# Kernel optimization log

Measured on AMD Instinct MI355X. Metric: run time of the kernel, lower is better.

Reference implementation:

```python
import jax, jax.numpy as jnp
import numpy as np

H = 16          # hidden_size
L = 24          # num_layers
LEN_TRAIN = 96
LEN_PRED = 48
B = 256         # leading dim of input (acts as TIME axis for the LSTMs, see notes)


def setup_inputs() -> dict:
    key = jax.random.key(0)
    ks = jax.random.split(key, 16)
    s = 1.0 / np.sqrt(H)  # PyTorch LSTM/Linear init scale
    u = lambda k, shp: jax.random.uniform(k, shp, jnp.float32, -s, s)
    return {
        "x": jax.random.normal(ks[0], (B, 1, LEN_TRAIN), jnp.float32),
        # lstm1: layer0 input_size=1, layers 1..23 input_size=2H
        "W_ih0_1": u(ks[1], (2, 4 * H, 1)),
        "W_ih_1": u(ks[2], (L - 1, 2, 4 * H, 2 * H)),
        "W_hh_1": u(ks[3], (L, 2, 4 * H, H)),
        "b_ih_1": u(ks[4], (L, 2, 4 * H)),
        "b_hh_1": u(ks[5], (L, 2, 4 * H)),
        # lstm2: all layers input_size=2H
        "W_ih_2": u(ks[6], (L, 2, 4 * H, 2 * H)),
        "W_hh_2": u(ks[7], (L, 2, 4 * H, H)),
        "b_ih_2": u(ks[8], (L, 2, 4 * H)),
        "b_hh_2": u(ks[9], (L, 2, 4 * H)),
        "fc1_w": u(ks[10], (1000, 2 * LEN_PRED * H)),
        "fc1_b": u(ks[11], (1000,)),
        "fc2_w": u(ks[12], (LEN_PRED, 1000)),
        "fc2_b": u(ks[13], (LEN_PRED,)),
    }


def _lstm_dir(x, Wih, Whh, bih, bhh, reverse):
    # x: (T, N, in). Precompute input-gate GEMM over whole sequence.
    xg = jnp.einsum("tni,gi->tng", x, Wih) + bih + bhh  # (T, N, 4H)

    def step(carry, g_in):
        h, c = carry
        g = g_in + h @ Whh.T
        i, f, gg, o = jnp.split(g, 4, axis=-1)  # PyTorch gate order i,f,g,o
        c = jax.nn.sigmoid(f) * c + jax.nn.sigmoid(i) * jnp.tanh(gg)
        h = jax.nn.sigmoid(o) * jnp.tanh(c)
        return (h, c), h

    N = x.shape[1]
    init = (jnp.zeros((N, H), x.dtype), jnp.zeros((N, H), x.dtype))
    _, hs = jax.lax.scan(step, init, xg, reverse=reverse)
    return hs  # (T, N, H), in original time order


def _bilstm_stack(x, Wih_per_layer, Whh, bih, bhh):
    for l in range(Whh.shape[0]):
        Wih = Wih_per_layer[l]
        fwd = _lstm_dir(x, Wih[0], Whh[l, 0], bih[l, 0], bhh[l, 0], False)
        bwd = _lstm_dir(x, Wih[1], Whh[l, 1], bih[l, 1], bhh[l, 1], True)
        x = jnp.concatenate([fwd, bwd], axis=-1)  # (T, N, 2H)
    return x


def reference(x, W_ih0_1, W_ih_1, W_hh_1, b_ih_1, b_hh_1,
              W_ih_2, W_hh_2, b_ih_2, b_hh_2,
              fc1_w, fc1_b, fc2_w, fc2_b):
    xp = jnp.transpose(x, (0, 2, 1))  # (B, 96, 1); dim0 is the LSTM time axis (batch_first=False quirk)
    wih1 = [W_ih0_1] + [W_ih_1[i] for i in range(L - 1)]
    h = _bilstm_stack(xp, wih1, W_hh_1, b_ih_1, b_hh_1)      # (B, 96, 2H)
    x1 = h[:, -LEN_PRED:, :]                                  # (B, 48, 2H)
    wih2 = [W_ih_2[i] for i in range(L)]
    h2 = _bilstm_stack(x1, wih2, W_hh_2, b_ih_2, b_hh_2)      # (B, 48, 2H)
    z = h2 + x1
    flat = z.reshape(z.shape[0], -1)                          # (B, 1536)
    y = jax.nn.relu(flat @ fc1_w.T + fc1_b) @ fc2_w.T + fc2_b # (B, 48)
    return jnp.transpose(y.reshape(y.shape[0], LEN_PRED, 1), (0, 2, 1))  # (B, 1, 48)
```

## Files before the change

kernel.cpp:

```cpp
#include <hip/hip_runtime.h>


template <int SEL>
__device__ __forceinline__ float quad_bcast(float v) {
  return __int_as_float(__builtin_amdgcn_update_dpp(
      0, __float_as_int(v), SEL * 0x55, 0xF, 0xF, true));
}

__global__ __launch_bounds__(512) void lstm_fused(
    const float* __restrict__ x, const float* __restrict__ W_ih0_1,
    const float* __restrict__ W_ih_1, const float* __restrict__ W_hh_1,
    const float* __restrict__ b_ih_1, const float* __restrict__ b_hh_1,
    const float* __restrict__ W_ih_2, const float* __restrict__ W_hh_2,
    const float* __restrict__ b_ih_2, const float* __restrict__ b_hh_2,
    float* __restrict__ x1out, float* __restrict__ h2out) {
  __shared__ float xgF[256 * 64];
  __shared__ float xgB[256 * 64];

  const int tid = threadIdx.x;
  const int lane = tid & 63;
  const int w = tid >> 6;
  const int np = blockIdx.x;
  const int nglob = 48 + np;

  {
    const int d = w >> 2;
    const int wv = w & 3;
    float* xg = d ? xgB : xgF;
    const int r = lane;
    const float bias = b_ih_1[d * 64 + r] + b_hh_1[d * 64 + r];
    const float wih0 = W_ih0_1[d * 64 + r];
    const int xvb = __float_as_int(x[(size_t)(wv * 64 + lane) * 96 + nglob]);
    for (int ti = 0; ti < 64; ++ti) {
      const float xs = __int_as_float(__builtin_amdgcn_readlane(xvb, ti));
      xg[(wv * 64 + ti) * 64 + r] = fmaf(wih0, xs, bias);
    }
  }
  __syncthreads();

  for (int L = 0; L < 48; ++L) {
    float wf[32], wb[32];
    float bf0, bf1, bb0, bb1;
    {
      const int M = (L < 47) ? (L + 1) : 47;
      const float* WihP;
      const float* bihP;
      const float* bhhP;
      if (M < 24) {
        WihP = W_ih_1 + (size_t)(M - 1) * 4096;
        bihP = b_ih_1 + (size_t)M * 128;
        bhhP = b_hh_1 + (size_t)M * 128;
      } else {
        WihP = W_ih_2 + (size_t)(M - 24) * 4096;
        bihP = b_ih_2 + (size_t)(M - 24) * 128;
        bhhP = b_hh_2 + (size_t)(M - 24) * 128;
      }
      const int r = lane;
      bf0 = bihP[r];
      bf1 = bhhP[r];
      bb0 = bihP[64 + r];
      bb1 = bhhP[64 + r];
      const float4* pf = reinterpret_cast<const float4*>(WihP + (size_t)r * 32);
      const float4* pb =
          reinterpret_cast<const float4*>(WihP + 2048 + (size_t)r * 32);
#pragma unroll
      for (int q = 0; q < 8; ++q) {
        const float4 a = pf[q];
        wf[4 * q + 0] = a.x;
        wf[4 * q + 1] = a.y;
        wf[4 * q + 2] = a.z;
        wf[4 * q + 3] = a.w;
        const float4 b = pb[q];
        wb[4 * q + 0] = b.x;
        wb[4 * q + 1] = b.y;
        wb[4 * q + 2] = b.z;
        wb[4 * q + 3] = b.w;
      }
    }

    if (w == 0 || w == 5) {
      const int d = (w == 5);
      float* xg = d ? xgB : xgF;
      const int j = lane >> 2;
      const int g = lane & 3;
      const int r = g * 16 + j;

      const float* WhhP = ((L < 24) ? (W_hh_1 + (size_t)L * 2048)
                                    : (W_hh_2 + (size_t)(L - 24) * 2048)) +
                          (size_t)d * 1024 + (size_t)r * 16;
      float whh[16];
#pragma unroll
      for (int k = 0; k < 16; ++k) whh[k] = WhhP[k];

      const float s_ = (g == 2) ? 2.885390082f : -1.442695041f;
      const float m_ = (g == 2) ? -2.0f : 1.0f;
      const float b_ = (g == 2) ? 1.0f : 0.0f;

      float hs[16];
#pragma unroll
      for (int k = 0; k < 16; ++k) hs[k] = 0.f;
      float c = 0.f;

      const int dt = d ? -1 : 1;
      int t = d ? 255 : 0;
      float cur0 = xg[t * 64 + r];
      float cur1 = xg[(t + dt) * 64 + r];

#define LSTM_STEP(CUR, TT)                                                  \
  {                                                                         \
    float a0 = (CUR), a1 = 0.f, a2 = 0.f, a3 = 0.f;                         \
    _Pragma("unroll") for (int k = 0; k < 16; k += 4) {                     \
      a0 = fmaf(whh[k + 0], hs[k + 0], a0);                                 \
      a1 = fmaf(whh[k + 1], hs[k + 1], a1);                                 \
      a2 = fmaf(whh[k + 2], hs[k + 2], a2);                                 \
      a3 = fmaf(whh[k + 3], hs[k + 3], a3);                                 \
    }                                                                       \
    const float gv = (a0 + a1) + (a2 + a3);                                 \
    const float e = __builtin_amdgcn_exp2f(s_ * gv);                        \
    const float v = fmaf(m_, __builtin_amdgcn_rcpf(1.0f + e), b_);          \
    const float si = quad_bcast<0>(v);                                      \
    const float sf = quad_bcast<1>(v);                                      \
    const float tg = quad_bcast<2>(v);                                      \
    const float so = quad_bcast<3>(v);                                      \
    c = fmaf(sf, c, si * tg);                                               \
    const float e2 = __builtin_amdgcn_exp2f(2.885390082f * c);              \
    const float th = fmaf(-2.0f, __builtin_amdgcn_rcpf(1.0f + e2), 1.0f);   \
    const float h = so * th;                                                \
    xg[(TT)*64 + r] = h;  \
    const int hb = __float_as_int(h);                                       \
    _Pragma("unroll") for (int k = 0; k < 16; ++k) hs[k] =                  \
        __int_as_float(__builtin_amdgcn_readlane(hb, 4 * k));               \
  }

      for (int tt = 0; tt < 256; tt += 2) {
        const float nx0 = xg[((t + 2 * dt) & 255) * 64 + r];
        LSTM_STEP(cur0, t)
        const float nx1 = xg[((t + 3 * dt) & 255) * 64 + r];
        LSTM_STEP(cur1, t + dt)
        cur0 = nx0;
        cur1 = nx1;
        t += 2 * dt;
      }
#undef LSTM_STEP
    }
    __syncthreads();

    if (L == 23 || L == 47) {
      float* dst = (L == 23) ? x1out : h2out;
#pragma unroll
      for (int p = 0; p < 4; ++p) {
        const int gi = p * 512 + tid;
        const int t = gi >> 3;
        const int cc = gi & 7;
        const float* src =
            (cc < 4) ? &xgF[t * 64 + cc * 4] : &xgB[t * 64 + (cc - 4) * 4];
        const float4 v = *reinterpret_cast<const float4*>(src);
        *reinterpret_cast<float4*>(dst + ((size_t)t * 48 + np) * 32 + cc * 4) =
            v;
      }
      if (L == 47) break;
      __syncthreads();
    }

    {
      const float biasF = bf0 + bf1;
      const float biasB = bb0 + bb1;

      float4 nf[4], nb[4];
      {
        const float4* qf = reinterpret_cast<const float4*>(&xgF[(w * 32) * 64]);
        const float4* qb = reinterpret_cast<const float4*>(&xgB[(w * 32) * 64]);
#pragma unroll
        for (int q = 0; q < 4; ++q) {
          nf[q] = qf[q];
          nb[q] = qb[q];
        }
      }
      for (int ti = 0; ti < 32; ++ti) {
        const int t = w * 32 + ti;
        float xv[32];
#pragma unroll
        for (int q = 0; q < 4; ++q) {
          const float4 a = nf[q];
          xv[4 * q + 0] = a.x;
          xv[4 * q + 1] = a.y;
          xv[4 * q + 2] = a.z;
          xv[4 * q + 3] = a.w;
          const float4 b = nb[q];
          xv[16 + 4 * q + 0] = b.x;
          xv[16 + 4 * q + 1] = b.y;
          xv[16 + 4 * q + 2] = b.z;
          xv[16 + 4 * q + 3] = b.w;
        }
        if (ti < 31) {
          const float4* qf =
              reinterpret_cast<const float4*>(&xgF[(t + 1) * 64]);
          const float4* qb =
              reinterpret_cast<const float4*>(&xgB[(t + 1) * 64]);
#pragma unroll
          for (int q = 0; q < 4; ++q) {
            nf[q] = qf[q];
            nb[q] = qb[q];
          }
        }
        float f0 = biasF, f1 = 0.f, f2 = 0.f, f3 = 0.f;
        float g0 = biasB, g1 = 0.f, g2 = 0.f, g3 = 0.f;
#pragma unroll
        for (int k = 0; k < 32; k += 4) {
          f0 = fmaf(wf[k + 0], xv[k + 0], f0);
          f1 = fmaf(wf[k + 1], xv[k + 1], f1);
          f2 = fmaf(wf[k + 2], xv[k + 2], f2);
          f3 = fmaf(wf[k + 3], xv[k + 3], f3);
          g0 = fmaf(wb[k + 0], xv[k + 0], g0);
          g1 = fmaf(wb[k + 1], xv[k + 1], g1);
          g2 = fmaf(wb[k + 2], xv[k + 2], g2);
          g3 = fmaf(wb[k + 3], xv[k + 3], g3);
        }
        xgF[t * 64 + lane] = (f0 + f1) + (f2 + f3);
        xgB[t * 64 + lane] = (g0 + g1) + (g2 + g3);
      }
    }
    __syncthreads();
  }
}

__global__ __launch_bounds__(256) void fc1_kernel(
    const float* __restrict__ h2, const float* __restrict__ x1b,
    const float* __restrict__ w1, const float* __restrict__ b1,
    float* __restrict__ y1) {
  __shared__ float Zs[16][68];
  __shared__ float Ws[16][68];
  const int tid = threadIdx.x;
  const int m0 = blockIdx.x * 64;
  const int b0 = blockIdx.y * 64;
  const int rr = tid >> 2;
  const int c4 = (tid & 3) * 4;
  const int tx = tid & 15, ty = tid >> 4;

  float acc[4][4];
#pragma unroll
  for (int i = 0; i < 4; ++i)
#pragma unroll
    for (int jj = 0; jj < 4; ++jj) acc[i][jj] = 0.f;

  const bool wvalid = (m0 + rr) < 1000;
  const float* zr = h2 + (size_t)(b0 + rr) * 1536 + c4;
  const float* zr2 = x1b + (size_t)(b0 + rr) * 1536 + c4;
  const float* wr = w1 + (size_t)(m0 + rr) * 1536 + c4;

  float4 za = *reinterpret_cast<const float4*>(zr);
  float4 zb = *reinterpret_cast<const float4*>(zr2);
  float4 wv = wvalid ? *reinterpret_cast<const float4*>(wr)
                     : make_float4(0.f, 0.f, 0.f, 0.f);

  for (int k0 = 0; k0 < 1536; k0 += 16) {
    Zs[c4 + 0][rr] = za.x + zb.x;
    Zs[c4 + 1][rr] = za.y + zb.y;
    Zs[c4 + 2][rr] = za.z + zb.z;
    Zs[c4 + 3][rr] = za.w + zb.w;
    Ws[c4 + 0][rr] = wv.x;
    Ws[c4 + 1][rr] = wv.y;
    Ws[c4 + 2][rr] = wv.z;
    Ws[c4 + 3][rr] = wv.w;
    if (k0 + 16 < 1536) {
      za = *reinterpret_cast<const float4*>(zr + k0 + 16);
      zb = *reinterpret_cast<const float4*>(zr2 + k0 + 16);
      if (wvalid) wv = *reinterpret_cast<const float4*>(wr + k0 + 16);
    }
    __syncthreads();
#pragma unroll
    for (int kk = 0; kk < 16; ++kk) {
      const float4 av = *reinterpret_cast<const float4*>(&Zs[kk][ty * 4]);
      const float4 bv = *reinterpret_cast<const float4*>(&Ws[kk][tx * 4]);
      const float a_[4] = {av.x, av.y, av.z, av.w};
      const float b_[4] = {bv.x, bv.y, bv.z, bv.w};
#pragma unroll
      for (int i = 0; i < 4; ++i)
#pragma unroll
        for (int jj = 0; jj < 4; ++jj)
          acc[i][jj] = fmaf(a_[i], b_[jj], acc[i][jj]);
    }
    __syncthreads();
  }
#pragma unroll
  for (int i = 0; i < 4; ++i) {
    const int b = b0 + ty * 4 + i;
#pragma unroll
    for (int jj = 0; jj < 4; ++jj) {
      const int m = m0 + tx * 4 + jj;
      if (m < 1000) {
        float vo = acc[i][jj] + b1[m];
        y1[(size_t)b * 1000 + m] = vo > 0.f ? vo : 0.f;
      }
    }
  }
}

__global__ __launch_bounds__(64) void fc2_kernel(
    const float* __restrict__ y1, const float* __restrict__ w2,
    const float* __restrict__ b2, float* __restrict__ out) {
  __shared__ float ys[1000];
  const int b = blockIdx.x;
  for (int k = threadIdx.x; k < 1000; k += 64) ys[k] = y1[(size_t)b * 1000 + k];
  __syncthreads();
  const int p = threadIdx.x;
  if (p < 48) {
    float a0 = b2[p], a1 = 0.f, a2 = 0.f, a3 = 0.f;
    const float* wr = w2 + (size_t)p * 1000;
    for (int k = 0; k < 1000; k += 4) {
      const float4 wv = *reinterpret_cast<const float4*>(wr + k);
      a0 = fmaf(ys[k + 0], wv.x, a0);
      a1 = fmaf(ys[k + 1], wv.y, a1);
      a2 = fmaf(ys[k + 2], wv.z, a2);
      a3 = fmaf(ys[k + 3], wv.w, a3);
    }
    out[(size_t)b * 48 + p] = (a0 + a1) + (a2 + a3);
  }
}

extern "C" void kernel_launch(void* const* d_in, const int* in_sizes, int n_in,
                              void* d_out, int out_size, void* d_ws,
                              size_t ws_size, hipStream_t stream) {
  const float* x = (const float*)d_in[0];
  const float* W_ih0_1 = (const float*)d_in[1];
  const float* W_ih_1 = (const float*)d_in[2];
  const float* W_hh_1 = (const float*)d_in[3];
  const float* b_ih_1 = (const float*)d_in[4];
  const float* b_hh_1 = (const float*)d_in[5];
  const float* W_ih_2 = (const float*)d_in[6];
  const float* W_hh_2 = (const float*)d_in[7];
  const float* b_ih_2 = (const float*)d_in[8];
  const float* b_hh_2 = (const float*)d_in[9];
  const float* fc1_w = (const float*)d_in[10];
  const float* fc1_b = (const float*)d_in[11];
  const float* fc2_w = (const float*)d_in[12];
  const float* fc2_b = (const float*)d_in[13];

  float* ws = (float*)d_ws;
  float* x1b = ws;
  float* h2b = ws + 393216;
  float* y1 = ws + 786432;

  lstm_fused<<<48, 512, 0, stream>>>(x, W_ih0_1, W_ih_1, W_hh_1, b_ih_1,
                                     b_hh_1, W_ih_2, W_hh_2, b_ih_2, b_hh_2,
                                     x1b, h2b);
  fc1_kernel<<<dim3(16, 4), 256, 0, stream>>>(h2b, x1b, fc1_w, fc1_b, y1);
  fc2_kernel<<<256, 64, 0, stream>>>(y1, fc2_w, fc2_b, (float*)d_out);
}
```

Baseline: 2.495 ms.

## Overlap next-layer input projection with recurrent tail and prescale gate constants

The recurrence for each layer is split into a 192-step segment and a final 64-step segment. While the recurrent waves finish the last 64 steps, other waves compute the next layer's input-gate projection for the middle time rows that both directions have already finished. Activation scale factors are folded into the stored input gates and the recurrent weights, which removes multiplies from the serial step, and next-layer W_hh is prefetched into registers. This adds an extra barrier per layer and more register pressure, and priority is raised on the recurrent waves to keep the critical path fast.

```diff
diff --git a/kernel.cpp b/kernel.cpp
--- a/kernel.cpp
+++ b/kernel.cpp
@@ -23,24 +23,56 @@
   const int np = blockIdx.x;
   const int nglob = 48 + np;
 
+  const bool rec = (w == 0) || (w == 5);
+  const int d = (w == 5) ? 1 : 0;
+
+  const float srowA =
+      ((lane >> 4) == 2) ? 2.885390082f : -1.442695041f;
+
   {
-    const int d = w >> 2;
+    const int dd = w >> 2;
     const int wv = w & 3;
-    float* xg = d ? xgB : xgF;
-    const int r = lane;
-    const float bias = b_ih_1[d * 64 + r] + b_hh_1[d * 64 + r];
-    const float wih0 = W_ih0_1[d * 64 + r];
+    float* xg = dd ? xgB : xgF;
+    const float bias =
+        (b_ih_1[dd * 64 + lane] + b_hh_1[dd * 64 + lane]) * srowA;
+    const float wih0 = W_ih0_1[dd * 64 + lane] * srowA;
     const int xvb = __float_as_int(x[(size_t)(wv * 64 + lane) * 96 + nglob]);
     for (int ti = 0; ti < 64; ++ti) {
       const float xs = __int_as_float(__builtin_amdgcn_readlane(xvb, ti));
-      xg[(wv * 64 + ti) * 64 + r] = fmaf(wih0, xs, bias);
-    }
+      xg[(wv * 64 + ti) * 64 + lane] = fmaf(wih0, xs, bias);
+    }
+  }
+
+  int jj = 0, g = 0, r = 0;
+  float s_ = 0.f, m_ = 0.f, b_ = 0.f;
+  float whn[16];
+  if (rec) {
+    jj = lane >> 2;
+    g = lane & 3;
+    r = g * 16 + jj;
+    s_ = (g == 2) ? 2.885390082f : -1.442695041f;
+    m_ = (g == 2) ? -5.770780164f : 1.0f;
+    b_ = (g == 2) ? 2.885390082f : 0.0f;
+    const float* W0 = W_hh_1 + (size_t)d * 1024 + (size_t)r * 16;
+#pragma unroll
+    for (int k = 0; k < 16; ++k) whn[k] = W0[k];
   }
   __syncthreads();
 
   for (int L = 0; L < 48; ++L) {
-    float wf[32], wb[32];
-    float bf0, bf1, bb0, bb1;
+    float whc[16];
+    if (rec) {
+#pragma unroll
+      for (int k = 0; k < 16; ++k) whc[k] = whn[k] * s_;
+      const int M = (L < 47) ? (L + 1) : 47;
+      const float* Wn = ((M < 24) ? (W_hh_1 + (size_t)M * 2048)
+                                  : (W_hh_2 + (size_t)(M - 24) * 2048)) +
+                        (size_t)d * 1024 + (size_t)r * 16;
+#pragma unroll
+      for (int k = 0; k < 16; ++k) whn[k] = Wn[k];
+    }
+
+    float wf[32], wb[32], bf, bb;
     {
       const int M = (L < 47) ? (L + 1) : 47;
       const float* WihP;
@@ -55,14 +87,12 @@
         bihP = b_ih_2 + (size_t)(M - 24) * 128;
         bhhP = b_hh_2 + (size_t)(M - 24) * 128;
       }
-      const int r = lane;
-      bf0 = bihP[r];
-      bf1 = bhhP[r];
-      bb0 = bihP[64 + r];
-      bb1 = bhhP[64 + r];
-      const float4* pf = reinterpret_cast<const float4*>(WihP + (size_t)r * 32);
+      bf = bihP[lane] + bhhP[lane];
+      bb = bihP[64 + lane] + bhhP[64 + lane];
+      const float4* pf =
+          reinterpret_cast<const float4*>(WihP + (size_t)lane * 32);
       const float4* pb =
-          reinterpret_cast<const float4*>(WihP + 2048 + (size_t)r * 32);
+          reinterpret_cast<const float4*>(WihP + 2048 + (size_t)lane * 32);
 #pragma unroll
       for (int q = 0; q < 8; ++q) {
         const float4 a = pf[q];
@@ -78,106 +108,19 @@
       }
     }
 
-    if (w == 0 || w == 5) {
-      const int d = (w == 5);
-      float* xg = d ? xgB : xgF;
-      const int j = lane >> 2;
-      const int g = lane & 3;
-      const int r = g * 16 + j;
-
-      const float* WhhP = ((L < 24) ? (W_hh_1 + (size_t)L * 2048)
-                                    : (W_hh_2 + (size_t)(L - 24) * 2048)) +
-                          (size_t)d * 1024 + (size_t)r * 16;
-      float whh[16];
-#pragma unroll
-      for (int k = 0; k < 16; ++k) whh[k] = WhhP[k];
-
-      const float s_ = (g == 2) ? 2.885390082f : -1.442695041f;
-      const float m_ = (g == 2) ? -2.0f : 1.0f;
-      const float b_ = (g == 2) ? 1.0f : 0.0f;
-
-      float hs[16];
-#pragma unroll
-      for (int k = 0; k < 16; ++k) hs[k] = 0.f;
-      float c = 0.f;
-
-      const int dt = d ? -1 : 1;
-      int t = d ? 255 : 0;
-      float cur0 = xg[t * 64 + r];
-      float cur1 = xg[(t + dt) * 64 + r];
-
-#define LSTM_STEP(CUR, TT)                                                  \
-  {                                                                         \
-    float a0 = (CUR), a1 = 0.f, a2 = 0.f, a3 = 0.f;                         \
-    _Pragma("unroll") for (int k = 0; k < 16; k += 4) {                     \
-      a0 = fmaf(whh[k + 0], hs[k + 0], a0);                                 \
-      a1 = fmaf(whh[k + 1], hs[k + 1], a1);                                 \
-      a2 = fmaf(whh[k + 2], hs[k + 2], a2);                                 \
-      a3 = fmaf(whh[k + 3], hs[k + 3], a3);                                 \
-    }                                                                       \
-    const float gv = (a0 + a1) + (a2 + a3);                                 \
-    const float e = __builtin_amdgcn_exp2f(s_ * gv);                        \
-    const float v = fmaf(m_, __builtin_amdgcn_rcpf(1.0f + e), b_);          \
-    const float si = quad_bcast<0>(v);                                      \
-    const float sf = quad_bcast<1>(v);                                      \
-    const float tg = quad_bcast<2>(v);                                      \
-    const float so = quad_bcast<3>(v);                                      \
-    c = fmaf(sf, c, si * tg);                                               \
-    const float e2 = __builtin_amdgcn_exp2f(2.885390082f * c);              \
-    const float th = fmaf(-2.0f, __builtin_amdgcn_rcpf(1.0f + e2), 1.0f);   \
-    const float h = so * th;                                                \
-    xg[(TT)*64 + r] = h;  \
-    const int hb = __float_as_int(h);                                       \
-    _Pragma("unroll") for (int k = 0; k < 16; ++k) hs[k] =                  \
-        __int_as_float(__builtin_amdgcn_readlane(hb, 4 * k));               \
-  }
-
-      for (int tt = 0; tt < 256; tt += 2) {
-        const float nx0 = xg[((t + 2 * dt) & 255) * 64 + r];
-        LSTM_STEP(cur0, t)
-        const float nx1 = xg[((t + 3 * dt) & 255) * 64 + r];
-        LSTM_STEP(cur1, t + dt)
-        cur0 = nx0;
-        cur1 = nx1;
-        t += 2 * dt;
-      }
-#undef LSTM_STEP
-    }
-    __syncthreads();
-
-    if (L == 23 || L == 47) {
-      float* dst = (L == 23) ? x1out : h2out;
-#pragma unroll
-      for (int p = 0; p < 4; ++p) {
-        const int gi = p * 512 + tid;
-        const int t = gi >> 3;
-        const int cc = gi & 7;
-        const float* src =
-            (cc < 4) ? &xgF[t * 64 + cc * 4] : &xgB[t * 64 + (cc - 4) * 4];
-        const float4 v = *reinterpret_cast<const float4*>(src);
-        *reinterpret_cast<float4*>(dst + ((size_t)t * 48 + np) * 32 + cc * 4) =
-            v;
-      }
-      if (L == 47) break;
-      __syncthreads();
-    }
-
-    {
-      const float biasF = bf0 + bf1;
-      const float biasB = bb0 + bb1;
-
+    auto phaseA_rows = [&](int t0, int cnt) {
       float4 nf[4], nb[4];
       {
-        const float4* qf = reinterpret_cast<const float4*>(&xgF[(w * 32) * 64]);
-        const float4* qb = reinterpret_cast<const float4*>(&xgB[(w * 32) * 64]);
+        const float4* qf = reinterpret_cast<const float4*>(&xgF[t0 * 64]);
+        const float4* qb = reinterpret_cast<const float4*>(&xgB[t0 * 64]);
 #pragma unroll
         for (int q = 0; q < 4; ++q) {
           nf[q] = qf[q];
           nb[q] = qb[q];
         }
       }
-      for (int ti = 0; ti < 32; ++ti) {
-        const int t = w * 32 + ti;
+      for (int i = 0; i < cnt; ++i) {
+        const int t = t0 + i;
         float xv[32];
 #pragma unroll
         for (int q = 0; q < 4; ++q) {
@@ -192,7 +135,7 @@
           xv[16 + 4 * q + 2] = b.z;
           xv[16 + 4 * q + 3] = b.w;
         }
-        if (ti < 31) {
+        if (i + 1 < cnt) {
           const float4* qf =
               reinterpret_cast<const float4*>(&xgF[(t + 1) * 64]);
           const float4* qb =
@@ -203,8 +146,8 @@
             nb[q] = qb[q];
           }
         }
-        float f0 = biasF, f1 = 0.f, f2 = 0.f, f3 = 0.f;
-        float g0 = biasB, g1 = 0.f, g2 = 0.f, g3 = 0.f;
+        float f0 = bf, f1 = 0.f, f2 = 0.f, f3 = 0.f;
+        float g0 = bb, g1 = 0.f, g2 = 0.f, g3 = 0.f;
 #pragma unroll
         for (int k = 0; k < 32; k += 4) {
           f0 = fmaf(wf[k + 0], xv[k + 0], f0);
@@ -216,9 +159,97 @@
           g2 = fmaf(wb[k + 2], xv[k + 2], g2);
           g3 = fmaf(wb[k + 3], xv[k + 3], g3);
         }
-        xgF[t * 64 + lane] = (f0 + f1) + (f2 + f3);
-        xgB[t * 64 + lane] = (g0 + g1) + (g2 + g3);
-      }
+        xgF[t * 64 + lane] = ((f0 + f1) + (f2 + f3)) * srowA;
+        xgB[t * 64 + lane] = ((g0 + g1) + (g2 + g3)) * srowA;
+      }
+    };
+
+    float hs[16];
+    float c = 0.f;
+    int t = d ? 255 : 0;
+    const int dt = d ? -1 : 1;
+    float cur0 = 0.f, cur1 = 0.f;
+    float* xg = d ? xgB : xgF;
+
+#define LSTM_STEP(CUR, TT)                                                  \
+  {                                                                         \
+    float a0 = (CUR), a1 = 0.f, a2 = 0.f, a3 = 0.f;                         \
+    _Pragma("unroll") for (int k = 0; k < 16; k += 4) {                     \
+      a0 = fmaf(whc[k + 0], hs[k + 0], a0);                                 \
+      a1 = fmaf(whc[k + 1], hs[k + 1], a1);                                 \
+      a2 = fmaf(whc[k + 2], hs[k + 2], a2);                                 \
+      a3 = fmaf(whc[k + 3], hs[k + 3], a3);                                 \
+    }                                                                       \
+    const float gv = (a0 + a1) + (a2 + a3);                                 \
+    const float e = __builtin_amdgcn_exp2f(gv);                             \
+    const float v = fmaf(m_, __builtin_amdgcn_rcpf(1.0f + e), b_);          \
+    const float si = quad_bcast<0>(v);                                      \
+    const float sf = quad_bcast<1>(v);                                      \
+    const float tg = quad_bcast<2>(v);                  \
+    const float so = quad_bcast<3>(v);                                      \
+    c = fmaf(sf, c, si * tg);                  \
+    const float e2 = __builtin_amdgcn_exp2f(c);                             \
+    const float th = fmaf(-2.0f, __builtin_amdgcn_rcpf(1.0f + e2), 1.0f);   \
+    const float h = so * th;                                                \
+    xg[(TT)*64 + r] = h;  \
+    const int hb = __float_as_int(h);                                       \
+    _Pragma("unroll") for (int k = 0; k < 16; ++k) hs[k] =                  \
+        __int_as_float(__builtin_amdgcn_readlane(hb, 4 * k));               \
+  }
+
+    auto run_steps = [&](int nsteps) {
+      for (int tt = 0; tt < nsteps; tt += 2) {
+        const float nx0 = xg[((t + 2 * dt) & 255) * 64 + r];
+        LSTM_STEP(cur0, t)
+        const float nx1 = xg[((t + 3 * dt) & 255) * 64 + r];
+        LSTM_STEP(cur1, t + dt)
+        cur0 = nx0;
+        cur1 = nx1;
+        t += 2 * dt;
+      }
+    };
+
+    if (rec) {
+#pragma unroll
+      for (int k = 0; k < 16; ++k) hs[k] = 0.f;
+      cur0 = xg[t * 64 + r];
+      cur1 = xg[(t + dt) * 64 + r];
+      run_steps(192);
+    }
+    __syncthreads();
+
+    if (rec) {
+      __builtin_amdgcn_s_setprio(1);
+      run_steps(64);
+      __builtin_amdgcn_s_setprio(0);
+    } else if (w == 2 || w == 3 || w == 6 || w == 7) {
+      if (L != 23 && L != 47) {
+        const int widx = ((w >> 2) << 1) | (w & 1);
+        phaseA_rows(64 + widx * 32, 32);
+      }
+    }
+#undef LSTM_STEP
+    __syncthreads();
+
+    if (L == 23 || L == 47) {
+      float* dst = (L == 23) ? x1out : h2out;
+#pragma unroll
+      for (int p = 0; p < 4; ++p) {
+        const int gi = p * 512 + tid;
+        const int tt = gi >> 3;
+        const int cc = gi & 7;
+        const float* src =
+            (cc < 4) ? &xgF[tt * 64 + cc * 4] : &xgB[tt * 64 + (cc - 4) * 4];
+        const float4 v = *reinterpret_cast<const float4*>(src);
+        *reinterpret_cast<float4*>(dst + ((size_t)tt * 48 + np) * 32 +
+                                   cc * 4) = v;
+      }
+      if (L == 47) break;
+      __syncthreads();
+      phaseA_rows(w * 32, 32);
+    } else {
+      const int t0 = (w < 4) ? (w * 16) : (192 + (w - 4) * 16);
+      phaseA_rows(t0, 16);
     }
     __syncthreads();
   }
```

Result: slower. 3.239 ms (+29.8%).
